# Optimization experiments

Measured on AMD Instinct MI355X. Metric: run time of the kernel, lower is better.

The kernel has to match this reference:

```python
import jax, jax.numpy as jnp
import numpy as np

B, N, S, D1, D2 = 4, 16384, 4096, 128, 256
C_IN = D1 + D2  # 384
MLP = [256, 256]
EPS_BN = 1e-5


def setup_inputs() -> dict:
    key = jax.random.key(0)
    ks = jax.random.split(key, 16)
    inp = {
        "points_xyz1": jax.random.normal(ks[0], (B, N, 3), dtype=jnp.float32),
        "points_xyz2": jax.random.normal(ks[1], (B, S, 3), dtype=jnp.float32),
        "points_fea1": jax.random.normal(ks[2], (B, D1, N), dtype=jnp.float32),
        "points_fea2": jax.random.normal(ks[3], (B, D2, S), dtype=jnp.float32),
    }
    c_in = C_IN
    for i, c_out in enumerate(MLP):
        scale = 1.0 / np.sqrt(c_in)
        inp[f"W{i}"] = jax.random.uniform(ks[4 + 3 * i], (c_out, c_in), jnp.float32, -scale, scale)
        inp[f"b{i}"] = jax.random.uniform(ks[5 + 3 * i], (c_out,), jnp.float32, -scale, scale)
        inp[f"gamma{i}"] = jnp.ones((c_out,), jnp.float32)
        inp[f"beta{i}"] = jnp.zeros((c_out,), jnp.float32)
        c_in = c_out
    return inp


def _coordinate_distance(x1, x2):
    # squared euclidean distance matrix: (B,N,S)
    n1 = jnp.sum(x1 * x1, axis=-1, keepdims=True)          # (B,N,1)
    n2 = jnp.sum(x2 * x2, axis=-1, keepdims=True)          # (B,S,1)
    return n1 + jnp.swapaxes(n2, 1, 2) - 2.0 * jnp.einsum("bnc,bsc->bns", x1, x2)


def _conv_bn_relu(x, W, b, gamma, beta):
    # 1x1 conv: (B,Cin,N) -> (B,Cout,N), then BatchNorm1d (training stats) + ReLU
    y = jnp.einsum("oc,bcn->bon", W, x) + b[None, :, None]
    mean = jnp.mean(y, axis=(0, 2), keepdims=True)
    var = jnp.var(y, axis=(0, 2), keepdims=True)
    y = (y - mean) * jax.lax.rsqrt(var + EPS_BN)
    y = y * gamma[None, :, None] + beta[None, :, None]
    return jax.nn.relu(y)


def reference(points_xyz1, points_xyz2, points_fea1, points_fea2,
              W0, b0, gamma0, beta0, W1, b1, gamma1, beta1):
    dists = _coordinate_distance(points_xyz1[..., :3], points_xyz2[..., :3])  # (B,N,S)
    neg_d, idx = jax.lax.top_k(-dists, 3)                                     # 3 smallest
    d3 = -neg_d                                                               # (B,N,3)
    dist_recip = 1.0 / jnp.maximum(d3, 1e-8)
    weight = dist_recip / jnp.sum(dist_recip, axis=2, keepdims=True)          # (B,N,3)
    fea2t = jnp.swapaxes(points_fea2, 1, 2)                                   # (B,S,D2)
    gathered = fea2t[jnp.arange(B)[:, None, None], idx]                       # (B,N,3,D2)
    interp = jnp.sum(gathered * weight[..., None], axis=2)                    # (B,N,D2)
    new_fea = jnp.concatenate((points_fea1, jnp.swapaxes(interp, 1, 2)), axis=1)  # (B,D1+D2,N)
    new_fea = _conv_bn_relu(new_fea, W0, b0, gamma0, beta0)
    new_fea = _conv_bn_relu(new_fea, W1, b1, gamma1, beta1)
    return new_fea
```

## Files before the change

### kernel.cpp

```cpp
#include <hip/hip_runtime.h>
#include <math.h>

namespace {

constexpr int kB = 4;
constexpr int kN = 16384;
constexpr int kS = 4096;
constexpr int kD1 = 128;
constexpr int kD2 = 256;
constexpr int kCO = 256;
constexpr int kNCOL = kB * kN;
constexpr int kKX = kD1 + kD2;

constexpr size_t kOffAb0  = 262144;
constexpr size_t kOffAb1  = 264192;
constexpr size_t kOffX1p  = 266240;
constexpr size_t kOffPart = 33820672;

typedef __bf16 bf16x8 __attribute__((ext_vector_type(8)));
typedef float f32x4 __attribute__((ext_vector_type(4)));

__device__ __forceinline__ float bf2f(unsigned short u) {
  unsigned int x = ((unsigned int)u) << 16;
  float f;
  __builtin_memcpy(&f, &x, 4);
  return f;
}
__device__ __forceinline__ unsigned short f2bf(float f) {
  unsigned int x;
  __builtin_memcpy(&x, &f, 4);
  x += 0x7fffu + ((x >> 16) & 1u);
  return (unsigned short)(x >> 16);
}

__device__ __forceinline__ void cp16_async(const void* g, void* l) {
#if __has_builtin(__builtin_amdgcn_global_load_lds)
  __builtin_amdgcn_global_load_lds(
      (const __attribute__((address_space(1))) unsigned int*)g,
      (__attribute__((address_space(3))) unsigned int*)l, 16, 0, 0);
#else
  *(uint4*)l = *(const uint4*)g;
#endif
}

__global__ __launch_bounds__(256) void pts4_kernel(const float* __restrict__ xyz2,
                                                   float4* __restrict__ pts4) {
#pragma clang fp contract(off)
  int i = blockIdx.x * 256 + threadIdx.x;
  float x = xyz2[i * 3 + 0];
  float y = xyz2[i * 3 + 1];
  float z = xyz2[i * 3 + 2];
  float4 p;
  p.w = (x * x + y * y) + z * z;
  p.x = x + x; p.y = y + y; p.z = z + z;
  pts4[i] = p;
}

__global__ __launch_bounds__(256) void transpose_kernel(const float* __restrict__ fea2,
                                                        float* __restrict__ fea2t) {
  __shared__ float T[64][65];
  int b = blockIdx.z;
  int c0 = blockIdx.y * 64;
  int s0 = blockIdx.x * 64;
  int t = threadIdx.x;
  {
    int sl = t & 63, cg2 = t >> 6;
#pragma unroll
    for (int i = 0; i < 16; ++i) {
      int cl = cg2 * 16 + i;
      T[sl][cl] = fea2[((size_t)(b * kD2 + c0 + cl)) * kS + s0 + sl];
    }
  }
  __syncthreads();
  {
    int cl = t & 63, sg = t >> 6;
#pragma unroll
    for (int i = 0; i < 16; ++i) {
      int sl = sg * 16 + i;
      fea2t[((size_t)(b * kS + s0 + sl)) * kD2 + c0 + cl] = T[sl][cl];
    }
  }
}

__global__ __launch_bounds__(256) void fea1t_kernel(const float* __restrict__ fea1,
                                                    unsigned short* __restrict__ XT) {
  __shared__ float T[64][129];
  int n0 = blockIdx.x * 64;
  int b = blockIdx.y;
  int t = threadIdx.x;
  {
    int nl = t & 63, cg2 = t >> 6;
#pragma unroll
    for (int i = 0; i < 32; ++i) {
      int c = cg2 * 32 + i;
      T[nl][c] = fea1[((size_t)(b * kD1 + c)) * kN + n0 + nl];
    }
  }
  __syncthreads();
  {
    int nl = t >> 2, ch = t & 3;
    unsigned short h[32];
#pragma unroll
    for (int i = 0; i < 32; ++i) h[i] = f2bf(T[nl][ch * 32 + i]);
    uint4* dst = (uint4*)&XT[(size_t)(b * kN + n0 + nl) * kKX + ch * 32];
#pragma unroll
    for (int i = 0; i < 4; ++i) dst[i] = ((uint4*)h)[i];
  }
}

__global__ __launch_bounds__(512) void knn_interp_kernel(
    const float* __restrict__ xyz1, const float4* __restrict__ pts4,
    const float* __restrict__ fea2t, unsigned short* __restrict__ XT) {
#pragma clang fp contract(off)
  __shared__ float cd[8][64][3];
  __shared__ int ci[8][64][3];
  __shared__ float wsh[3][64];
  __shared__ int ish[3][64];
  int tid = threadIdx.x;
  int q = tid & 63;
  int chunk = __builtin_amdgcn_readfirstlane(tid >> 6);
  int b = blockIdx.x >> 8;
  int n0 = (blockIdx.x & 255) * 64;
  int n = n0 + q;
  int qg = b * kN + n;

  const float* p1 = xyz1 + (size_t)qg * 3;
  float x = p1[0], y = p1[1], z = p1[2];
  float n1 = (x * x + y * y) + z * z;

  const float4* pp = pts4 + b * kS + chunk * 512;
  int sbase = chunk * 512;
  float d0v = 1e30f, d1v = 1e30f, d2v = 1e30f;
  int i0 = 0, i1 = 0, i2 = 0;
  for (int s = 0; s < 512; s += 4) {
    float4 P[4];
    P[0] = pp[s]; P[1] = pp[s + 1]; P[2] = pp[s + 2]; P[3] = pp[s + 3];
#pragma unroll
    for (int u = 0; u < 4; ++u) {
      float dot2 = (x * P[u].x + y * P[u].y) + z * P[u].z;
      float d = (n1 + P[u].w) - dot2;
      if (__ballot(d < d2v)) {
        int si = sbase + s + u;
        bool b0 = d < d0v, b1 = d < d1v, b2 = d < d2v;
        int i2n = b1 ? i1 : (b2 ? si : i2);
        int i1n = b0 ? i0 : (b1 ? si : i1);
        int i0n = b0 ? si : i0;
        d2v = __builtin_amdgcn_fmed3f(d1v, d, d2v);
        d1v = __builtin_amdgcn_fmed3f(d0v, d, d1v);
        d0v = fminf(d0v, d);
        i0 = i0n; i1 = i1n; i2 = i2n;
      }
    }
  }
  cd[chunk][q][0] = d0v; cd[chunk][q][1] = d1v; cd[chunk][q][2] = d2v;
  ci[chunk][q][0] = i0;  ci[chunk][q][1] = i1;  ci[chunk][q][2] = i2;
  __syncthreads();

  if (tid < 64) {
    float D0 = 1e30f, D1 = 1e30f, D2 = 1e30f;
    int I0 = -1, I1 = -1, I2 = -1;
    for (int c2 = 0; c2 < 8; ++c2) {
#pragma unroll
      for (int k = 0; k < 3; ++k) {
        float d = cd[c2][tid][k];
        int i = ci[c2][tid][k];
        bool q0 = (d < D0) || (d == D0 && i < I0);
        bool q1 = (d < D1) || (d == D1 && i < I1);
        bool q2 = (d < D2) || (d == D2 && i < I2);
        if (q0)      { D2 = D1; I2 = I1; D1 = D0; I1 = I0; D0 = d; I0 = i; }
        else if (q1) { D2 = D1; I2 = I1; D1 = d;  I1 = i; }
        else if (q2) { D2 = d;  I2 = i; }
      }
    }
    float r0 = 1.0f / fmaxf(D0, 1e-8f);
    float r1 = 1.0f / fmaxf(D1, 1e-8f);
    float r2 = 1.0f / fmaxf(D2, 1e-8f);
    float rs = (r0 + r1) + r2;
    wsh[0][tid] = r0 / rs; wsh[1][tid] = r1 / rs; wsh[2][tid] = r2 / rs;
    ish[0][tid] = I0; ish[1][tid] = I1; ish[2][tid] = I2;
  }
  __syncthreads();

  int gq = tid >> 3, l = tid & 7;
  float w0 = wsh[0][gq], w1 = wsh[1][gq], w2 = wsh[2][gq];
  int qg2 = b * kN + n0 + gq;
  const float* fb = fea2t + ((size_t)b * kS) * kD2;
  const float* g0p = fb + (size_t)ish[0][gq] * kD2;
  const float* g1p = fb + (size_t)ish[1][gq] * kD2;
  const float* g2p = fb + (size_t)ish[2][gq] * kD2;
  unsigned short* op = XT + (size_t)qg2 * kKX + kD1;
#pragma unroll
  for (int k = 0; k < 8; ++k) {
    int c = (l + 8 * k) * 4;
    float4 f0 = *(const float4*)(g0p + c);
    float4 f1 = *(const float4*)(g1p + c);
    float4 f2 = *(const float4*)(g2p + c);
    unsigned short h[4];
    h[0] = f2bf((w0 * f0.x + w1 * f1.x) + w2 * f2.x);
    h[1] = f2bf((w0 * f0.y + w1 * f1.y) + w2 * f2.y);
    h[2] = f2bf((w0 * f0.z + w1 * f1.z) + w2 * f2.z);
    h[3] = f2bf((w0 * f0.w + w1 * f1.w) + w2 * f2.w);
    *(uint2*)(op + c) = *(uint2*)h;
  }
}

__global__ __launch_bounds__(256) void gemm0t_kernel(
    const float* __restrict__ W, const unsigned short* __restrict__ Bt,
    const float* __restrict__ bias, unsigned short* __restrict__ X1pre,
    float* __restrict__ partS, float* __restrict__ partQ) {
  constexpr int KDIM = kKX;
  constexpr int ALD = 40;
  __shared__ unsigned short smem[9216];
  unsigned short* As = smem;
  unsigned short* Bs = smem + 128 * ALD;
  __shared__ float psum[2][128], pq[2][128];
  int tid = threadIdx.x;
  int j0 = blockIdx.x * 128;
  int m0 = blockIdx.y * 128;
  int w = tid >> 6, lane = tid & 63;
  int wm = w & 1, wn = w >> 1;
  int quad = lane >> 4, l16 = lane & 15;
  int arow = tid & 127, ahalf = tid >> 7;
  int brow = tid >> 2, bch = tid & 3;

  bf16x8 pone, pm;
#pragma unroll
  for (int i = 0; i < 8; ++i) { pone[i] = (__bf16)1.0f; pm[i] = (__bf16)(float)l16; }
  f32x4 zf = {};
  f32x4 dr = __builtin_amdgcn_mfma_f32_16x16x32_bf16(pm, pone, zf, 0, 0, 0);
  f32x4 dc = __builtin_amdgcn_mfma_f32_16x16x32_bf16(pone, pm, zf, 0, 0, 0);
  int rowv[4], colv[4];
#pragma unroll
  for (int r = 0; r < 4; ++r) {
    rowv[r] = (int)(dr[r] * (1.0f / 32.0f) + 0.5f);
    colv[r] = (int)(dc[r] * (1.0f / 32.0f) + 0.5f);
  }

  f32x4 acc[4][4] = {};
  for (int k0 = 0; k0 < KDIM; k0 += 32) {
    cp16_async(Bt + (size_t)(j0 + brow) * KDIM + k0 + bch * 8, &Bs[(size_t)tid * 8]);
    cp16_async(Bt + (size_t)(j0 + 64 + brow) * KDIM + k0 + bch * 8, &Bs[(size_t)(tid + 256) * 8]);
    {
      const float* ap = W + (size_t)(m0 + arow) * KDIM + k0 + ahalf * 16;
      float4 f0 = *(const float4*)(ap);
      float4 f1 = *(const float4*)(ap + 4);
      float4 f2 = *(const float4*)(ap + 8);
      float4 f3 = *(const float4*)(ap + 12);
      unsigned short h[16] = {f2bf(f0.x), f2bf(f0.y), f2bf(f0.z), f2bf(f0.w),
                              f2bf(f1.x), f2bf(f1.y), f2bf(f1.z), f2bf(f1.w),
                              f2bf(f2.x), f2bf(f2.y), f2bf(f2.z), f2bf(f2.w),
                              f2bf(f3.x), f2bf(f3.y), f2bf(f3.z), f2bf(f3.w)};
      uint4* dst = (uint4*)&As[arow * ALD + ahalf * 16];
      dst[0] = ((uint4*)h)[0];
      dst[1] = ((uint4*)h)[1];
    }
    __syncthreads();
    bf16x8 af[4], bfr[4];
#pragma unroll
    for (int mt = 0; mt < 4; ++mt)
      af[mt] = *(const bf16x8*)(&As[(wm * 64 + mt * 16 + l16) * ALD + quad * 8]);
#pragma unroll
    for (int nt = 0; nt < 4; ++nt)
      bfr[nt] = *(const bf16x8*)(&Bs[(wn * 64 + nt * 16 + l16) * 32 + quad * 8]);
#pragma unroll
    for (int mt = 0; mt < 4; ++mt)
#pragma unroll
      for (int nt = 0; nt < 4; ++nt)
        acc[mt][nt] = __builtin_amdgcn_mfma_f32_16x16x32_bf16(af[mt], bfr[nt], acc[mt][nt], 0, 0, 0);
    __syncthreads();
  }

  uint2 h2[4][4];
#pragma unroll
  for (int mt = 0; mt < 4; ++mt) {
    int obase = m0 + wm * 64 + mt * 16 + rowv[0];
    float4 bv4 = *(const float4*)&bias[obase];
    float s4[4] = {0.f, 0.f, 0.f, 0.f}, q4[4] = {0.f, 0.f, 0.f, 0.f};
#pragma unroll
    for (int nt = 0; nt < 4; ++nt) {
      unsigned short hh[4];
#pragma unroll
      for (int r = 0; r < 4; ++r) {
        float v = acc[mt][nt][r] + ((const float*)&bv4)[r];
        s4[r] += v; q4[r] += v * v;
        hh[r] = f2bf(v);
      }
      h2[mt][nt] = *(uint2*)hh;
    }
#pragma unroll
    for (int r = 0; r < 4; ++r) {
      float s = s4[r], qq = q4[r];
#pragma unroll
      for (int d2 = 1; d2 < 16; d2 <<= 1) {
        s += __shfl_xor(s, d2, 64);
        qq += __shfl_xor(qq, d2, 64);
      }
      if (l16 == 0) {
        int ol = wm * 64 + mt * 16 + rowv[0] + r;
        psum[wn][ol] = s;
        pq[wn][ol] = qq;
      }
    }
  }

  unsigned short* T = smem + wm * 4608;
  int jr = lane >> 3, cc = lane & 7;
  if (wn == 0) {
#pragma unroll
    for (int mt = 0; mt < 4; ++mt)
#pragma unroll
      for (int nt = 0; nt < 4; ++nt)
        *(uint2*)&T[(nt * 16 + colv[0]) * 72 + mt * 16 + rowv[0]] = h2[mt][nt];
#pragma unroll
    for (int it = 0; it < 8; ++it) {
      int jl = it * 8 + jr;
      uint4 u = *(uint4*)&T[jl * 72 + cc * 8];
      *(uint4*)&X1pre[(size_t)(j0 + jl) * kCO + m0 + wm * 64 + cc * 8] = u;
    }
  }
  __syncthreads();
  if (wn == 1) {
#pragma unroll
    for (int mt = 0; mt < 4; ++mt)
#pragma unroll
      for (int nt = 0; nt < 4; ++nt)
        *(uint2*)&T[(nt * 16 + colv[0]) * 72 + mt * 16 + rowv[0]] = h2[mt][nt];
#pragma unroll
    for (int it = 0; it < 8; ++it) {
      int jl = it * 8 + jr;
      uint4 u = *(uint4*)&T[jl * 72 + cc * 8];
      *(uint4*)&X1pre[(size_t)(j0 + 64 + jl) * kCO + m0 + wm * 64 + cc * 8] = u;
    }
  }
  if (tid < 128) {
    float ss = psum[0][tid] + psum[1][tid];
    float qq = pq[0][tid] + pq[1][tid];
    partS[(size_t)blockIdx.x * kCO + m0 + tid] = ss;
    partQ[(size_t)blockIdx.x * kCO + m0 + tid] = qq;
  }
}

__global__ __launch_bounds__(64) void redstats_kernel(
    const float* __restrict__ pS, const float* __restrict__ pQ,
    const float* __restrict__ gamma, const float* __restrict__ beta,
    float* __restrict__ ab) {
  int o = blockIdx.x, t = threadIdx.x;
  float s = 0.f, q = 0.f;
  for (int i = t; i < 512; i += 64) {
    s += pS[(size_t)i * kCO + o];
    q += pQ[(size_t)i * kCO + o];
  }
#pragma unroll
  for (int d = 1; d < 64; d <<= 1) {
    s += __shfl_xor(s, d, 64);
    q += __shfl_xor(q, d, 64);
  }
  if (t == 0) {
    float m = s * (1.0f / 65536.f);
    float var = q * (1.0f / 65536.f) - m * m;
    float rsq = 1.0f / sqrtf(var + 1e-5f);
    float a = gamma[o] * rsq;
    ab[o] = a;
    ab[kCO + o] = beta[o] - m * a;
  }
}

__global__ __launch_bounds__(256) void gemm1f_kernel(
    const float* __restrict__ W, const unsigned short* __restrict__ Xp,
    const float* __restrict__ bias, const float* __restrict__ ab0,
    float* __restrict__ out, float* __restrict__ partS, float* __restrict__ partQ) {
  constexpr int KDIM = kCO;
  constexpr int ALD = 40;
  __shared__ unsigned short As[128 * ALD];
  __shared__ unsigned short Bs[128 * 32];
  __shared__ float Acf[256], Ccf[256];
  __shared__ float psum[2][128], pq[2][128];
  int tid = threadIdx.x;
  int j0 = blockIdx.x * 128;
  int m0 = blockIdx.y * 128;
  int w = tid >> 6, lane = tid & 63;
  int wm = w & 1, wn = w >> 1;
  int quad = lane >> 4, l16 = lane & 15;
  int arow = tid & 127, ahalf = tid >> 7;
  int brow = tid >> 2, bch = tid & 3;

  if (tid < 256) { Acf[tid] = ab0[tid]; Ccf[tid] = ab0[kCO + tid]; }

  bf16x8 pone, pm;
#pragma unroll
  for (int i = 0; i < 8; ++i) { pone[i] = (__bf16)1.0f; pm[i] = (__bf16)(float)l16; }
  f32x4 zf = {};
  f32x4 dr = __builtin_amdgcn_mfma_f32_16x16x32_bf16(pm, pone, zf, 0, 0, 0);
  f32x4 dc = __builtin_amdgcn_mfma_f32_16x16x32_bf16(pone, pm, zf, 0, 0, 0);
  int rowv[4], colv[4];
#pragma unroll
  for (int r = 0; r < 4; ++r) {
    rowv[r] = (int)(dr[r] * (1.0f / 32.0f) + 0.5f);
    colv[r] = (int)(dc[r] * (1.0f / 32.0f) + 0.5f);
  }
  __syncthreads();

  f32x4 acc[4][4] = {};
  for (int k0 = 0; k0 < KDIM; k0 += 32) {
    {
      int cb = k0 + bch * 8;
      float4 a0 = *(const float4*)&Acf[cb];
      float4 a1 = *(const float4*)&Acf[cb + 4];
      float4 c0 = *(const float4*)&Ccf[cb];
      float4 c1 = *(const float4*)&Ccf[cb + 4];
#pragma unroll
      for (int h = 0; h < 2; ++h) {
        uint4 raw = *(const uint4*)(Xp + (size_t)(j0 + h * 64 + brow) * kCO + cb);
        const unsigned short* rs = (const unsigned short*)&raw;
        unsigned short o8[8];
        o8[0] = f2bf(fmaxf(fmaf(a0.x, bf2f(rs[0]), c0.x), 0.f));
        o8[1] = f2bf(fmaxf(fmaf(a0.y, bf2f(rs[1]), c0.y), 0.f));
        o8[2] = f2bf(fmaxf(fmaf(a0.z, bf2f(rs[2]), c0.z), 0.f));
        o8[3] = f2bf(fmaxf(fmaf(a0.w, bf2f(rs[3]), c0.w), 0.f));
        o8[4] = f2bf(fmaxf(fmaf(a1.x, bf2f(rs[4]), c1.x), 0.f));
        o8[5] = f2bf(fmaxf(fmaf(a1.y, bf2f(rs[5]), c1.y), 0.f));
        o8[6] = f2bf(fmaxf(fmaf(a1.z, bf2f(rs[6]), c1.z), 0.f));
        o8[7] = f2bf(fmaxf(fmaf(a1.w, bf2f(rs[7]), c1.w), 0.f));
        *(uint4*)&Bs[(size_t)(tid + h * 256) * 8] = *(uint4*)o8;
      }
    }
    {
      const float* ap = W + (size_t)(m0 + arow) * KDIM + k0 + ahalf * 16;
      float4 f0 = *(const float4*)(ap);
      float4 f1 = *(const float4*)(ap + 4);
      float4 f2 = *(const float4*)(ap + 8);
      float4 f3 = *(const float4*)(ap + 12);
      unsigned short h[16] = {f2bf(f0.x), f2bf(f0.y), f2bf(f0.z), f2bf(f0.w),
                              f2bf(f1.x), f2bf(f1.y), f2bf(f1.z), f2bf(f1.w),
                              f2bf(f2.x), f2bf(f2.y), f2bf(f2.z), f2bf(f2.w),
                              f2bf(f3.x), f2bf(f3.y), f2bf(f3.z), f2bf(f3.w)};
      uint4* dst = (uint4*)&As[arow * ALD + ahalf * 16];
      dst[0] = ((uint4*)h)[0];
      dst[1] = ((uint4*)h)[1];
    }
    __syncthreads();
    bf16x8 af[4], bfr[4];
#pragma unroll
    for (int mt = 0; mt < 4; ++mt)
      af[mt] = *(const bf16x8*)(&As[(wm * 64 + mt * 16 + l16) * ALD + quad * 8]);
#pragma unroll
    for (int nt = 0; nt < 4; ++nt)
      bfr[nt] = *(const bf16x8*)(&Bs[(wn * 64 + nt * 16 + l16) * 32 + quad * 8]);
#pragma unroll
    for (int mt = 0; mt < 4; ++mt)
#pragma unroll
      for (int nt = 0; nt < 4; ++nt)
        acc[mt][nt] = __builtin_amdgcn_mfma_f32_16x16x32_bf16(af[mt], bfr[nt], acc[mt][nt], 0, 0, 0);
    __syncthreads();
  }

#pragma unroll
  for (int mt = 0; mt < 4; ++mt) {
#pragma unroll
    for (int r = 0; r < 4; ++r) {
      int ol = wm * 64 + mt * 16 + rowv[r];
      int o = m0 + ol;
      float bv = bias[o];
      float s = 0.f, qq = 0.f;
#pragma unroll
      for (int nt = 0; nt < 4; ++nt) {
        int j = j0 + wn * 64 + nt * 16 + colv[r];
        float v = acc[mt][nt][r] + bv;
        s += v; qq += v * v;
        int bb = j >> 14, nn = j & (kN - 1);
        out[((size_t)(bb * kCO + o)) * kN + nn] = v;
      }
#pragma unroll
      for (int d2 = 1; d2 < 16; d2 <<= 1) {
        s += __shfl_xor(s, d2, 64);
        qq += __shfl_xor(qq, d2, 64);
      }
      if (l16 == 0) {
        psum[wn][ol] = s;
        pq[wn][ol] = qq;
      }
    }
  }
  __syncthreads();
  if (tid < 128) {
    float ss = psum[0][tid] + psum[1][tid];
    float qq = pq[0][tid] + pq[1][tid];
    partS[(size_t)blockIdx.x * kCO + m0 + tid] = ss;
    partQ[(size_t)blockIdx.x * kCO + m0 + tid] = qq;
  }
}

__global__ __launch_bounds__(256) void finalf_kernel(float* __restrict__ Y,
                                                     const float* __restrict__ ab) {
  size_t i = ((size_t)blockIdx.x * 256 + threadIdx.x) * 4;
  int o = (int)((i >> 14) & (kCO - 1));
  float a = ab[o], c = ab[kCO + o];
  float4 u = *(float4*)(Y + i);
  float* t = (float*)&u;
#pragma unroll
  for (int k = 0; k < 4; ++k) t[k] = fmaxf(fmaf(a, t[k], c), 0.0f);
  *(float4*)(Y + i) = u;
}

}

extern "C" void kernel_launch(void* const* d_in, const int* in_sizes, int n_in,
                              void* d_out, int out_size, void* d_ws, size_t ws_size,
                              hipStream_t stream) {
  const float* xyz1 = (const float*)d_in[0];
  const float* xyz2 = (const float*)d_in[1];
  const float* fea1 = (const float*)d_in[2];
  const float* fea2 = (const float*)d_in[3];
  const float* W0 = (const float*)d_in[4];
  const float* b0 = (const float*)d_in[5];
  const float* g0 = (const float*)d_in[6];
  const float* be0 = (const float*)d_in[7];
  const float* W1 = (const float*)d_in[8];
  const float* b1 = (const float*)d_in[9];
  const float* g1 = (const float*)d_in[10];
  const float* be1 = (const float*)d_in[11];
  float* out = (float*)d_out;

  char* ws = (char*)d_ws;
  float4* pts4 = (float4*)ws;
  float* ab0 = (float*)(ws + kOffAb0);
  float* ab1 = (float*)(ws + kOffAb1);
  unsigned short* X1pre = (unsigned short*)(ws + kOffX1p);
  float* partS = (float*)(ws + kOffPart);
  float* partQ = (float*)(ws + kOffPart + 524288);
  float* fea2t = (float*)(ws + kOffPart);
  unsigned short* XT = (unsigned short*)d_out;

  if (ws_size < (size_t)kOffPart + 2 * 524288) return;

  pts4_kernel<<<kB * kS / 256, 256, 0, stream>>>(xyz2, pts4);
  transpose_kernel<<<dim3(kS / 64, kD2 / 64, kB), 256, 0, stream>>>(fea2, fea2t);
  fea1t_kernel<<<dim3(kN / 64, kB), 256, 0, stream>>>(fea1, XT);
  knn_interp_kernel<<<kNCOL / 64, 512, 0, stream>>>(xyz1, pts4, fea2t, XT);
  gemm0t_kernel<<<dim3(kNCOL / 128, kCO / 128), 256, 0, stream>>>(W0, XT, b0, X1pre, partS, partQ);
  redstats_kernel<<<kCO, 64, 0, stream>>>(partS, partQ, g0, be0, ab0);
  gemm1f_kernel<<<dim3(kNCOL / 128, kCO / 128), 256, 0, stream>>>(W1, X1pre, b1, ab0, out, partS, partQ);
  redstats_kernel<<<kCO, 64, 0, stream>>>(partS, partQ, g1, be1, ab1);
  finalf_kernel<<<kCO * kNCOL / (256 * 4), 256, 0, stream>>>(out, ab1);
}
```

Baseline: 375.4 us.

## Fuse pts4 and fea2 transpose into one prep kernel; fold fea1 transpose into knn

```diff
diff --git a/kernel.cpp b/kernel.cpp
--- a/kernel.cpp
+++ b/kernel.cpp
@@ -43,26 +43,28 @@
 #endif
 }
 
-__global__ __launch_bounds__(256) void pts4_kernel(const float* __restrict__ xyz2,
-                                                   float4* __restrict__ pts4) {
+__global__ __launch_bounds__(256) void prep_kernel(const float* __restrict__ xyz2,
+                                                   float4* __restrict__ pts4,
+                                                   const float* __restrict__ fea2,
+                                                   float* __restrict__ fea2t) {
 #pragma clang fp contract(off)
-  int i = blockIdx.x * 256 + threadIdx.x;
-  float x = xyz2[i * 3 + 0];
-  float y = xyz2[i * 3 + 1];
-  float z = xyz2[i * 3 + 2];
-  float4 p;
-  p.w = (x * x + y * y) + z * z;
-  p.x = x + x; p.y = y + y; p.z = z + z;
-  pts4[i] = p;
-}
-
-__global__ __launch_bounds__(256) void transpose_kernel(const float* __restrict__ fea2,
-                                                        float* __restrict__ fea2t) {
+  int bid = blockIdx.x;
+  int t = threadIdx.x;
+  if (bid >= 1024) {
+    int i = (bid - 1024) * 256 + t;
+    float x = xyz2[i * 3 + 0];
+    float y = xyz2[i * 3 + 1];
+    float z = xyz2[i * 3 + 2];
+    float4 p;
+    p.w = (x * x + y * y) + z * z;
+    p.x = x + x; p.y = y + y; p.z = z + z;
+    pts4[i] = p;
+    return;
+  }
   __shared__ float T[64][65];
-  int b = blockIdx.z;
-  int c0 = blockIdx.y * 64;
-  int s0 = blockIdx.x * 64;
-  int t = threadIdx.x;
+  int s0 = (bid & 63) * 64;
+  int c0 = ((bid >> 6) & 3) * 64;
+  int b = bid >> 8;
   {
     int sl = t & 63, cg2 = t >> 6;
 #pragma unroll
@@ -82,40 +84,12 @@
   }
 }
 
-__global__ __launch_bounds__(256) void fea1t_kernel(const float* __restrict__ fea1,
-                                                    unsigned short* __restrict__ XT) {
-  __shared__ float T[64][129];
-  int n0 = blockIdx.x * 64;
-  int b = blockIdx.y;
-  int t = threadIdx.x;
-  {
-    int nl = t & 63, cg2 = t >> 6;
-#pragma unroll
-    for (int i = 0; i < 32; ++i) {
-      int c = cg2 * 32 + i;
-      T[nl][c] = fea1[((size_t)(b * kD1 + c)) * kN + n0 + nl];
-    }
-  }
-  __syncthreads();
-  {
-    int nl = t >> 2, ch = t & 3;
-    unsigned short h[32];
-#pragma unroll
-    for (int i = 0; i < 32; ++i) h[i] = f2bf(T[nl][ch * 32 + i]);
-    uint4* dst = (uint4*)&XT[(size_t)(b * kN + n0 + nl) * kKX + ch * 32];
-#pragma unroll
-    for (int i = 0; i < 4; ++i) dst[i] = ((uint4*)h)[i];
-  }
-}
-
 __global__ __launch_bounds__(512) void knn_interp_kernel(
     const float* __restrict__ xyz1, const float4* __restrict__ pts4,
-    const float* __restrict__ fea2t, unsigned short* __restrict__ XT) {
+    const float* __restrict__ fea2t, const float* __restrict__ fea1,
+    unsigned short* __restrict__ XT) {
 #pragma clang fp contract(off)
-  __shared__ float cd[8][64][3];
-  __shared__ int ci[8][64][3];
-  __shared__ float wsh[3][64];
-  __shared__ int ish[3][64];
+  __shared__ __align__(16) char lds_raw[33024];
   int tid = threadIdx.x;
   int q = tid & 63;
   int chunk = __builtin_amdgcn_readfirstlane(tid >> 6);
@@ -123,6 +97,30 @@
   int n0 = (blockIdx.x & 255) * 64;
   int n = n0 + q;
   int qg = b * kN + n;
+
+  {
+    float (*T)[129] = (float (*)[129])lds_raw;
+    int nl = tid & 63, cg2 = tid >> 6;
+#pragma unroll
+    for (int i = 0; i < 16; ++i) {
+      int c = cg2 * 16 + i;
+      T[nl][c] = fea1[((size_t)(b * kD1 + c)) * kN + n0 + nl];
+    }
+    __syncthreads();
+    int nl2 = tid >> 3, ch = tid & 7;
+    unsigned short h[16];
+#pragma unroll
+    for (int i = 0; i < 16; ++i) h[i] = f2bf(T[nl2][ch * 16 + i]);
+    uint4* dst = (uint4*)&XT[(size_t)(b * kN + n0 + nl2) * kKX + ch * 16];
+    dst[0] = ((uint4*)h)[0];
+    dst[1] = ((uint4*)h)[1];
+  }
+  __syncthreads();
+
+  float (*cd)[64][3] = (float (*)[64][3])lds_raw;
+  int   (*ci)[64][3] = (int (*)[64][3])(lds_raw + 6144);
+  float (*wsh)[64]   = (float (*)[64])(lds_raw + 12288);
+  int   (*ish)[64]   = (int (*)[64])(lds_raw + 13056);
 
   const float* p1 = xyz1 + (size_t)qg * 3;
   float x = p1[0], y = p1[1], z = p1[2];
@@ -533,10 +531,8 @@
 
   if (ws_size < (size_t)kOffPart + 2 * 524288) return;
 
-  pts4_kernel<<<kB * kS / 256, 256, 0, stream>>>(xyz2, pts4);
-  transpose_kernel<<<dim3(kS / 64, kD2 / 64, kB), 256, 0, stream>>>(fea2, fea2t);
-  fea1t_kernel<<<dim3(kN / 64, kB), 256, 0, stream>>>(fea1, XT);
-  knn_interp_kernel<<<kNCOL / 64, 512, 0, stream>>>(xyz1, pts4, fea2t, XT);
+  prep_kernel<<<1088, 256, 0, stream>>>(xyz2, pts4, fea2, fea2t);
+  knn_interp_kernel<<<kNCOL / 64, 512, 0, stream>>>(xyz1, pts4, fea2t, fea1, XT);
   gemm0t_kernel<<<dim3(kNCOL / 128, kCO / 128), 256, 0, stream>>>(W0, XT, b0, X1pre, partS, partQ);
   redstats_kernel<<<kCO, 64, 0, stream>>>(partS, partQ, g0, be0, ab0);
   gemm1f_kernel<<<dim3(kNCOL / 128, kCO / 128), 256, 0, stream>>>(W1, X1pre, b1, ab0, out, partS, partQ);
```

Result: no change. 380.4 us (+1.3%).

## Merge prep kernels, transpose BN partial layout, fold final stats into finalize

Applied to the files above, without the earlier changes.

```diff
diff --git a/kernel.cpp b/kernel.cpp
--- a/kernel.cpp
+++ b/kernel.cpp
@@ -13,7 +13,6 @@
 constexpr int kKX = kD1 + kD2;
 
 constexpr size_t kOffAb0  = 262144;
-constexpr size_t kOffAb1  = 264192;
 constexpr size_t kOffX1p  = 266240;
 constexpr size_t kOffPart = 33820672;
 
@@ -43,68 +42,72 @@
 #endif
 }
 
-__global__ __launch_bounds__(256) void pts4_kernel(const float* __restrict__ xyz2,
-                                                   float4* __restrict__ pts4) {
+__global__ __launch_bounds__(256) void prep_kernel(
+    const float* __restrict__ xyz2, float4* __restrict__ pts4,
+    const float* __restrict__ fea2, float* __restrict__ fea2t,
+    const float* __restrict__ fea1, unsigned short* __restrict__ XT) {
 #pragma clang fp contract(off)
-  int i = blockIdx.x * 256 + threadIdx.x;
-  float x = xyz2[i * 3 + 0];
-  float y = xyz2[i * 3 + 1];
-  float z = xyz2[i * 3 + 2];
-  float4 p;
-  p.w = (x * x + y * y) + z * z;
-  p.x = x + x; p.y = y + y; p.z = z + z;
-  pts4[i] = p;
-}
-
-__global__ __launch_bounds__(256) void transpose_kernel(const float* __restrict__ fea2,
-                                                        float* __restrict__ fea2t) {
-  __shared__ float T[64][65];
-  int b = blockIdx.z;
-  int c0 = blockIdx.y * 64;
-  int s0 = blockIdx.x * 64;
+  __shared__ __align__(16) char lds_raw[33024];
+  int bid = blockIdx.x;
   int t = threadIdx.x;
+  if (bid >= 1024 && bid < 1088) {
+    int i = (bid - 1024) * 256 + t;
+    float x = xyz2[i * 3 + 0];
+    float y = xyz2[i * 3 + 1];
+    float z = xyz2[i * 3 + 2];
+    float4 p;
+    p.w = (x * x + y * y) + z * z;
+    p.x = x + x; p.y = y + y; p.z = z + z;
+    pts4[i] = p;
+    return;
+  }
+  if (bid < 1024) {
+    float (*T)[65] = (float (*)[65])lds_raw;
+    int s0 = (bid & 63) * 64;
+    int c0 = ((bid >> 6) & 3) * 64;
+    int b = bid >> 8;
+    {
+      int sl = t & 63, cg2 = t >> 6;
+#pragma unroll
+      for (int i = 0; i < 16; ++i) {
+        int cl = cg2 * 16 + i;
+        T[sl][cl] = fea2[((size_t)(b * kD2 + c0 + cl)) * kS + s0 + sl];
+      }
+    }
+    __syncthreads();
+    {
+      int cl = t & 63, sg = t >> 6;
+#pragma unroll
+      for (int i = 0; i < 16; ++i) {
+        int sl = sg * 16 + i;
+        fea2t[((size_t)(b * kS + s0 + sl)) * kD2 + c0 + cl] = T[sl][cl];
+      }
+    }
+    return;
+  }
   {
-    int sl = t & 63, cg2 = t >> 6;
-#pragma unroll
-    for (int i = 0; i < 16; ++i) {
-      int cl = cg2 * 16 + i;
-      T[sl][cl] = fea2[((size_t)(b * kD2 + c0 + cl)) * kS + s0 + sl];
-    }
-  }
-  __syncthreads();
-  {
-    int cl = t & 63, sg = t >> 6;
-#pragma unroll
-    for (int i = 0; i < 16; ++i) {
-      int sl = sg * 16 + i;
-      fea2t[((size_t)(b * kS + s0 + sl)) * kD2 + c0 + cl] = T[sl][cl];
-    }
-  }
-}
-
-__global__ __launch_bounds__(256) void fea1t_kernel(const float* __restrict__ fea1,
-                                                    unsigned short* __restrict__ XT) {
-  __shared__ float T[64][129];
-  int n0 = blockIdx.x * 64;
-  int b = blockIdx.y;
-  int t = threadIdx.x;
-  {
-    int nl = t & 63, cg2 = t >> 6;
-#pragma unroll
-    for (int i = 0; i < 32; ++i) {
-      int c = cg2 * 32 + i;
-      T[nl][c] = fea1[((size_t)(b * kD1 + c)) * kN + n0 + nl];
-    }
-  }
-  __syncthreads();
-  {
-    int nl = t >> 2, ch = t & 3;
-    unsigned short h[32];
-#pragma unroll
-    for (int i = 0; i < 32; ++i) h[i] = f2bf(T[nl][ch * 32 + i]);
-    uint4* dst = (uint4*)&XT[(size_t)(b * kN + n0 + nl) * kKX + ch * 32];
-#pragma unroll
-    for (int i = 0; i < 4; ++i) dst[i] = ((uint4*)h)[i];
+    float (*T)[129] = (float (*)[129])lds_raw;
+    int fb = bid - 1088;
+    int n0 = (fb & 255) * 64;
+    int b = fb >> 8;
+    {
+      int nl = t & 63, cg2 = t >> 6;
+#pragma unroll
+      for (int i = 0; i < 32; ++i) {
+        int c = cg2 * 32 + i;
+        T[nl][c] = fea1[((size_t)(b * kD1 + c)) * kN + n0 + nl];
+      }
+    }
+    __syncthreads();
+    {
+      int nl = t >> 2, ch = t & 3;
+      unsigned short h[32];
+#pragma unroll
+      for (int i = 0; i < 32; ++i) h[i] = f2bf(T[nl][ch * 32 + i]);
+      uint4* dst = (uint4*)&XT[(size_t)(b * kN + n0 + nl) * kKX + ch * 32];
+#pragma unroll
+      for (int i = 0; i < 4; ++i) dst[i] = ((uint4*)h)[i];
+    }
   }
 }
 
@@ -335,8 +338,8 @@
   if (tid < 128) {
     float ss = psum[0][tid] + psum[1][tid];
     float qq = pq[0][tid] + pq[1][tid];
-    partS[(size_t)blockIdx.x * kCO + m0 + tid] = ss;
-    partQ[(size_t)blockIdx.x * kCO + m0 + tid] = qq;
+    partS[(size_t)(m0 + tid) * 512 + blockIdx.x] = ss;
+    partQ[(size_t)(m0 + tid) * 512 + blockIdx.x] = qq;
   }
 }
 
@@ -347,8 +350,8 @@
   int o = blockIdx.x, t = threadIdx.x;
   float s = 0.f, q = 0.f;
   for (int i = t; i < 512; i += 64) {
-    s += pS[(size_t)i * kCO + o];
-    q += pQ[(size_t)i * kCO + o];
+    s += pS[(size_t)o * 512 + i];
+    q += pQ[(size_t)o * 512 + i];
   }
 #pragma unroll
   for (int d = 1; d < 64; d <<= 1) {
@@ -485,21 +488,45 @@
   if (tid < 128) {
     float ss = psum[0][tid] + psum[1][tid];
     float qq = pq[0][tid] + pq[1][tid];
-    partS[(size_t)blockIdx.x * kCO + m0 + tid] = ss;
-    partQ[(size_t)blockIdx.x * kCO + m0 + tid] = qq;
-  }
-}
-
-__global__ __launch_bounds__(256) void finalf_kernel(float* __restrict__ Y,
-                                                     const float* __restrict__ ab) {
-  size_t i = ((size_t)blockIdx.x * 256 + threadIdx.x) * 4;
-  int o = (int)((i >> 14) & (kCO - 1));
-  float a = ab[o], c = ab[kCO + o];
-  float4 u = *(float4*)(Y + i);
+    partS[(size_t)(m0 + tid) * 512 + blockIdx.x] = ss;
+    partQ[(size_t)(m0 + tid) * 512 + blockIdx.x] = qq;
+  }
+}
+
+__global__ __launch_bounds__(256) void finalf_kernel(
+    float* __restrict__ Y, const float* __restrict__ pS,
+    const float* __restrict__ pQ, const float* __restrict__ gamma,
+    const float* __restrict__ beta) {
+  __shared__ float sw[4], qw[4], coef[2];
+  size_t base = (size_t)blockIdx.x * 1024;
+  int o = (int)((base >> 14) & (kCO - 1));
+  int tid = threadIdx.x;
+  float s = pS[(size_t)o * 512 + tid] + pS[(size_t)o * 512 + 256 + tid];
+  float q = pQ[(size_t)o * 512 + tid] + pQ[(size_t)o * 512 + 256 + tid];
+#pragma unroll
+  for (int d = 1; d < 64; d <<= 1) {
+    s += __shfl_xor(s, d, 64);
+    q += __shfl_xor(q, d, 64);
+  }
+  if ((tid & 63) == 0) { sw[tid >> 6] = s; qw[tid >> 6] = q; }
+  __syncthreads();
+  if (tid == 0) {
+    float st = (sw[0] + sw[1]) + (sw[2] + sw[3]);
+    float qt = (qw[0] + qw[1]) + (qw[2] + qw[3]);
+    float m = st * (1.0f / 65536.f);
+    float var = qt * (1.0f / 65536.f) - m * m;
+    float rsq = 1.0f / sqrtf(var + 1e-5f);
+    float a = gamma[o] * rsq;
+    coef[0] = a;
+    coef[1] = beta[o] - m * a;
+  }
+  __syncthreads();
+  float a = coef[0], c = coef[1];
+  float4 u = *(float4*)(Y + base + tid * 4);
   float* t = (float*)&u;
 #pragma unroll
   for (int k = 0; k < 4; ++k) t[k] = fmaxf(fmaf(a, t[k], c), 0.0f);
-  *(float4*)(Y + i) = u;
+  *(float4*)(Y + base + tid * 4) = u;
 }
 
 }
@@ -524,7 +551,6 @@
   char* ws = (char*)d_ws;
   float4* pts4 = (float4*)ws;
   float* ab0 = (float*)(ws + kOffAb0);
-  float* ab1 = (float*)(ws + kOffAb1);
   unsigned short* X1pre = (unsigned short*)(ws + kOffX1p);
   float* partS = (float*)(ws + kOffPart);
   float* partQ = (float*)(ws + kOffPart + 524288);
@@ -533,13 +559,10 @@
 
   if (ws_size < (size_t)kOffPart + 2 * 524288) return;
 
-  pts4_kernel<<<kB * kS / 256, 256, 0, stream>>>(xyz2, pts4);
-  transpose_kernel<<<dim3(kS / 64, kD2 / 64, kB), 256, 0, stream>>>(fea2, fea2t);
-  fea1t_kernel<<<dim3(kN / 64, kB), 256, 0, stream>>>(fea1, XT);
+  prep_kernel<<<2112, 256, 0, stream>>>(xyz2, pts4, fea2, fea2t, fea1, XT);
   knn_interp_kernel<<<kNCOL / 64, 512, 0, stream>>>(xyz1, pts4, fea2t, XT);
   gemm0t_kernel<<<dim3(kNCOL / 128, kCO / 128), 256, 0, stream>>>(W0, XT, b0, X1pre, partS, partQ);
   redstats_kernel<<<kCO, 64, 0, stream>>>(partS, partQ, g0, be0, ab0);
   gemm1f_kernel<<<dim3(kNCOL / 128, kCO / 128), 256, 0, stream>>>(W1, X1pre, b1, ab0, out, partS, partQ);
-  redstats_kernel<<<kCO, 64, 0, stream>>>(partS, partQ, g1, be1, ab1);
-  finalf_kernel<<<kCO * kNCOL / (256 * 4), 256, 0, stream>>>(out, ab1);
-}
+  finalf_kernel<<<kCO * kNCOL / (256 * 4), 256, 0, stream>>>(out, partS, partQ, g1, be1);
+}
```

Measured after the change: 370.8 us. No clear change (-1.2%).
